# Kernel tuning notes

Measured on AMD Instinct MI355X. Metric: run time of the kernel, lower is better.

The kernel has to match this reference:

```python
import jax, jax.numpy as jnp
import numpy as np

S, B, W, H = 97, 256, 1024, 16
HD = W // H


def setup_inputs() -> dict:
    key = jax.random.key(0)
    ks = jax.random.split(key, 16)
    def p(k, shape):
        return jax.random.normal(k, shape, jnp.float32) * 0.02
    return {
        "tensor": jax.random.normal(ks[0], (S, B, W), jnp.float32),
        "mask": jnp.zeros((S, S), jnp.float32),
        "q_w": p(ks[1], (W, W)), "q_b": p(ks[2], (W,)),
        "k_w": p(ks[3], (W, W)), "k_b": p(ks[4], (W,)),
        "v_w": p(ks[5], (W, W)), "v_b": p(ks[6], (W,)),
        "in_proj_w": p(ks[7], (3 * W, W)), "in_proj_b": p(ks[8], (3 * W,)),
        "mha_out_w": p(ks[9], (W, W)), "mha_out_b": p(ks[10], (W,)),
        "out_w": p(ks[11], (W, W)), "out_b": p(ks[12], (W,)),
    }


def _freqs_cos_sin(dim, seqlen, theta=10000.0):
    # matches precompute_freqs_cis: angle[t, j] = t / theta**(2j/dim)
    inv = 1.0 / (theta ** (jnp.arange(0, dim, 2, dtype=jnp.float32) / dim))  # (dim/2,)
    ang = jnp.arange(seqlen, dtype=jnp.float32)[:, None] * inv[None, :]      # (S, dim/2)
    return jnp.cos(ang)[:, None, :], jnp.sin(ang)[:, None, :]                # (S, 1, dim/2)


def _rotary(x, cos, sin):
    # x: (S, B, D); pairs (even, odd) along last dim form complex numbers
    s, b, d = x.shape
    xr = x.reshape(s, b, d // 2, 2)
    xe, xo = xr[..., 0], xr[..., 1]
    oe = xe * cos - xo * sin
    oo = xe * sin + xo * cos
    return jnp.stack([oe, oo], axis=-1).reshape(s, b, d)


def reference(tensor, mask, q_w, q_b, k_w, k_b, v_w, v_b,
              in_proj_w, in_proj_b, mha_out_w, mha_out_b, out_w, out_b):
    # tensor: (S, B, W) -- torch MHA default batch_first=False layout
    q = tensor @ q_w.T + q_b
    k = tensor @ k_w.T + k_b
    v = tensor @ v_w.T + v_b

    cos, sin = _freqs_cos_sin(W, S)
    q = _rotary(q, cos, sin)
    k = _rotary(k, cos, sin)

    # nn.MultiheadAttention internal in_proj (applied on top of q/k/v linears)
    Wq, Wk, Wv = in_proj_w[:W], in_proj_w[W:2 * W], in_proj_w[2 * W:]
    bq, bk, bv = in_proj_b[:W], in_proj_b[W:2 * W], in_proj_b[2 * W:]
    q = q @ Wq.T + bq
    k = k @ Wk.T + bk
    v = v @ Wv.T + bv

    def split_heads(x):  # (S,B,W) -> (B,H,S,HD)
        return x.reshape(S, B, H, HD).transpose(1, 2, 0, 3)

    qh, kh, vh = split_heads(q), split_heads(k), split_heads(v)
    scale = 1.0 / jnp.sqrt(jnp.float32(HD))
    scores = jnp.einsum('bhqd,bhkd->bhqk', qh, kh) * scale + mask  # additive float mask
    attn = jax.nn.softmax(scores, axis=-1)
    o = jnp.einsum('bhqk,bhkd->bhqd', attn, vh)      # (B,H,S,HD)
    o = o.transpose(2, 0, 1, 3).reshape(S, B, W)     # (S,B,W)
    o = o @ mha_out_w.T + mha_out_b                  # MHA out_proj
    return o @ out_w.T + out_b                       # module's final self.out
```

## Files before the change

### kernel.cpp

```cpp
#include <hip/hip_runtime.h>
#include <cstdint>
#include <cstddef>

#define S_LEN 97
#define B_DIM 256
#define W_DIM 1024
#define NH    16
#define HDIM  64
#define MROWS (S_LEN * B_DIM)

typedef unsigned short u16;
typedef __bf16 bf16x8 __attribute__((ext_vector_type(8)));
typedef float  f32x4  __attribute__((ext_vector_type(4)));

__device__ __forceinline__ u16 f2bf(float f) {
  __bf16 b = (__bf16)f;
  return __builtin_bit_cast(unsigned short, b);
}

__device__ __forceinline__ void gload16(const void* g, void* lds) {
  __builtin_amdgcn_global_load_lds(
      (const __attribute__((address_space(1))) void*)(uintptr_t)g,
      (__attribute__((address_space(3))) void*)(uint32_t)(uintptr_t)lds,
      16, 0, 0);
}

__global__ void k_misc(float* __restrict__ tab, const float* __restrict__ mask,
                       float* __restrict__ maskP, const float* __restrict__ q_b,
                       const float* __restrict__ k_b, float* __restrict__ bc1,
                       float* __restrict__ zb) {
  const int blk = blockIdx.x, t = threadIdx.x;
  if (blk < 194) {
    const int idx = blk * 256 + t;
    if (idx < S_LEN * 512) {
      const int s = idx / 512, i = idx % 512;
      const float freq = expf(-(float)i * (9.210340371976184f / 512.0f));
      float sv, cv;
      sincosf((float)s * freq, &sv, &cv);
      tab[idx * 2 + 0] = cv;
      tab[idx * 2 + 1] = sv;
    }
  } else if (blk < 258) {
    const int i = (blk - 194) * 256 + t;
    const int r = i >> 7, c = i & 127;
    float v;
    if (c >= S_LEN) v = -1e30f;
    else if (r < S_LEN) v = mask[r * S_LEN + c];
    else v = 0.f;
    maskP[i] = v;
  } else if (blk < 266) {
    const int i = (blk - 258) * 256 + t;
    bc1[i] = (i < W_DIM) ? q_b[i] : k_b[i - W_DIM];
  } else {
    const int i = (blk - 266) * 256 + t;
    zb[i] = 0.f;
  }
}

__global__ void k_wcvt(const float* __restrict__ q_w, const float* __restrict__ k_w,
                       const float* __restrict__ in_proj_w, const float* __restrict__ out_w,
                       u16* __restrict__ WC1, u16* __restrict__ W2, u16* __restrict__ WO) {
  const int i = blockIdx.x * 256 + threadIdx.x;
  const float* s; u16* d; int off;
  if (i < 262144)        { s = q_w;       d = WC1;           off = i; }
  else if (i < 524288)   { s = k_w;       d = WC1 + 1048576; off = i - 262144; }
  else if (i < 1310720)  { s = in_proj_w; d = W2;            off = i - 524288; }
  else                   { s = out_w;     d = WO;            off = i - 1310720; }
  float4 v = ((const float4*)s)[off];
  uint2 pk;
  pk.x = (uint32_t)f2bf(v.x) | ((uint32_t)f2bf(v.y) << 16);
  pk.y = (uint32_t)f2bf(v.z) | ((uint32_t)f2bf(v.w) << 16);
  ((uint2*)d)[off] = pk;
}

__global__ void k_cvt(const float* __restrict__ s, u16* __restrict__ d, int n4) {
  int i = blockIdx.x * blockDim.x + threadIdx.x;
  if (i >= n4) return;
  float4 v = ((const float4*)s)[i];
  uint2 pk;
  pk.x = (uint32_t)f2bf(v.x) | ((uint32_t)f2bf(v.y) << 16);
  pk.y = (uint32_t)f2bf(v.z) | ((uint32_t)f2bf(v.w) << 16);
  ((uint2*)d)[i] = pk;
}

__global__ void k_cvt_t2(const float* __restrict__ s0, u16* __restrict__ d0,
                         const float* __restrict__ s1, u16* __restrict__ d1) {
  __shared__ float t[32][33];
  const float* src = blockIdx.z ? s1 : s0;
  u16* dst = blockIdx.z ? d1 : d0;
  const int bx = blockIdx.x * 32, by = blockIdx.y * 32;
  const int tx = threadIdx.x, ty = threadIdx.y;
  for (int yy = ty; yy < 32; yy += 8)
    t[yy][tx] = src[(size_t)(by + yy) * 1024 + bx + tx];
  __syncthreads();
  for (int yy = ty; yy < 32; yy += 8)
    dst[(size_t)(bx + yy) * 1024 + by + tx] = f2bf(t[tx][yy]);
}

__global__ void k_biasfold2(const float* __restrict__ M0, const float* __restrict__ v0,
                            const float* __restrict__ b0, float* __restrict__ o0,
                            const float* __restrict__ M1, const float* __restrict__ v1,
                            const float* __restrict__ b1, float* __restrict__ o1) {
  const int blk = blockIdx.x;
  const int lane = threadIdx.x & 63, wave = threadIdx.x >> 6;
  const float* M; const float* v; const float* b2; float* out; int rb;
  if (blk < 256) { M = M0; v = v0; b2 = b0; out = o0; rb = blk * 4; }
  else           { M = M1; v = v1; b2 = b1; out = o1; rb = (blk - 256) * 4; }
  const int row = rb + wave;
  float s = 0.f;
  for (int k = lane; k < 1024; k += 64) s += M[(size_t)row * 1024 + k] * v[k];
#pragma unroll
  for (int d = 32; d; d >>= 1) s += __shfl_xor(s, d);
  if (lane == 0) out[row] = s + b2[row];
}

__global__ __launch_bounds__(256) void k_gemmfold(
    const u16* __restrict__ A0, const u16* __restrict__ B0, u16* __restrict__ C0,
    const u16* __restrict__ A1, const u16* __restrict__ B1, u16* __restrict__ C1,
    const float* __restrict__ zb) {
  __shared__ u16 As[128 * 64];
  __shared__ u16 Bs[128 * 64];

  const u16* A = blockIdx.z ? A1 : A0;
  const u16* Bw = blockIdx.z ? B1 : B0;
  u16* Cp = blockIdx.z ? C1 : C0;

  const int tid = threadIdx.x, lane = tid & 63, wave = tid >> 6;
  const int wm = wave >> 1, wn = wave & 1;
  const int m0 = blockIdx.y * 128;
  const int n0 = blockIdx.x * 128;

  f32x4 acc[4][4] = {};

  const int lrow = lane >> 3;
  const int lcol = (lane & 7) * 8;
  const u16* Ag = A + (size_t)(m0 + wave * 8 + lrow) * 1024 + lcol;
  const u16* Bg = Bw + (size_t)(n0 + wave * 8 + lrow) * 1024 + lcol;
  u16* Asl = As + wave * 8 * 64;
  u16* Bsl = Bs + wave * 8 * 64;

  for (int kt = 0; kt < 1024; kt += 64) {
#pragma unroll
    for (int i = 0; i < 4; ++i) {
      gload16(Ag + (size_t)(i * 32) * 1024 + kt, Asl + i * 2048);
      gload16(Bg + (size_t)(i * 32) * 1024 + kt, Bsl + i * 2048);
    }
    __syncthreads();
#pragma unroll
    for (int kk = 0; kk < 2; ++kk) {
      bf16x8 af[4], bfr[4];
#pragma unroll
      for (int m = 0; m < 4; ++m)
        af[m] = *(const bf16x8*)(As + (wm * 64 + m * 16 + (lane & 15)) * 64 + kk * 32 + (lane >> 4) * 8);
#pragma unroll
      for (int n = 0; n < 4; ++n)
        bfr[n] = *(const bf16x8*)(Bs + (wn * 64 + n * 16 + (lane & 15)) * 64 + kk * 32 + (lane >> 4) * 8);
#pragma unroll
      for (int m = 0; m < 4; ++m)
#pragma unroll
        for (int n = 0; n < 4; ++n)
          acc[m][n] = __builtin_amdgcn_mfma_f32_16x16x32_bf16(af[m], bfr[n], acc[m][n], 0, 0, 0);
    }
    __syncthreads();
  }

  const int r0 = (lane >> 4) * 4;
  const int c0 = lane & 15;
#pragma unroll
  for (int m = 0; m < 4; ++m)
#pragma unroll
    for (int n = 0; n < 4; ++n) {
      const int col = n0 + wn * 64 + n * 16 + c0;
#pragma unroll
      for (int r = 0; r < 4; ++r) {
        const int row = m0 + wm * 64 + m * 16 + r0 + r;
        Cp[(size_t)row * 1024 + col] = f2bf(acc[m][n][r] + zb[col]);
      }
    }
}

template <int MODE>
__global__ __launch_bounds__(512, 4) void k_gemm256(
    const u16* __restrict__ A, int lda,
    const u16* __restrict__ BwA, const u16* __restrict__ BwB,
    const float* __restrict__ biasA, const float* __restrict__ biasB,
    void* __restrict__ CpA, void* __restrict__ CpB, int ldc,
    size_t thirdStride, const float* __restrict__ tab, int Nt, int NtA) {
  __shared__ u16 lds[3 * 12288];

  const int tid = threadIdx.x, lane = tid & 63, wave = tid >> 6;
  const int wm = wave >> 2, wn = wave & 3;
  const int c0 = lane & 15, hi = lane >> 4;

  const int nwg = gridDim.x;
  const int qq = nwg >> 3, rr_ = nwg & 7;
  const int xcd = blockIdx.x & 7, sub = blockIdx.x >> 3;
  const int seq = (xcd < rr_ ? xcd * (qq + 1) : rr_ * (qq + 1) + (xcd - rr_) * qq) + sub;
  const int mt = seq / Nt, ntRaw = seq - mt * Nt;
  const int m0 = mt * 128;
  bool isV = false;
  int n0 = ntRaw * 256;
  const u16* Bbase;
  const float* bias;
  if (MODE == 0) {
    if (ntRaw >= NtA) {
      isV = true;
      n0 = (ntRaw - NtA) * 256;
      Bbase = BwB + (size_t)n0 * 1024;
      bias = biasB;
    } else {
      Bbase = BwA + (size_t)n0 * 1024;
      bias = biasA;
    }
  } else {
    Bbase = BwA + (size_t)n0 * 1024;
    bias = biasA;
  }
  const int aoff = (MODE == 1) ? (n0 & ~1023) : 0;

  const int Lb = tid >> 3, pc = tid & 7;
  const int lcl = pc ^ (Lb & 7);
  const int rsel = lcl >> 2;
  const int csel = (lcl & 3) * 8;
  const u16* aS = A + (size_t)(m0 + Lb + 64 * rsel) * lda + aoff + csel;
  const u16* bS0 = Bbase + (size_t)(Lb + 128 * rsel) * 1024 + csel;
  const u16* bS1 = Bbase + (size_t)(64 + Lb + 128 * rsel) * 1024 + csel;
  const uint32_t ldsW = wave * 512;

  auto stage = [&](int tt, u16* slot) {
    gload16(aS + tt * 32, slot + ldsW);
    gload16(bS0 + tt * 32, slot + 4096 + ldsW);
    gload16(bS1 + tt * 32, slot + 8192 + ldsW);
  };

  int aofr[4], bofr[4];
#pragma unroll
  for (int m = 0; m < 4; ++m)
    aofr[m] = (m * 16 + c0) * 64 + ((((wm << 2) | hi) ^ (c0 & 7)) * 8);
#pragma unroll
  for (int n = 0; n < 4; ++n)
    bofr[n] = 4096 + ((wn & 1) * 64 + n * 16 + c0) * 64 +
              (((((wn >> 1) << 2) | hi) ^ (c0 & 7)) * 8);

  u16* s0 = lds;
  u16* s1 = lds + 12288;
  u16* s2 = lds + 24576;

  stage(0, s0); stage(1, s1);
  asm volatile("s_waitcnt vmcnt(3)" ::: "memory");
  __builtin_amdgcn_s_barrier();
  __builtin_amdgcn_sched_barrier(0);

  f32x4 acc[4][4] = {};

  for (int t = 0; t < 32; ++t) {
    bf16x8 af[4], bfr[4];
#pragma unroll
    for (int n = 0; n < 4; ++n) bfr[n] = *(const bf16x8*)(s0 + bofr[n]);
#pragma unroll
    for (int m = 0; m < 4; ++m) af[m] = *(const bf16x8*)(s0 + aofr[m]);
    if (t + 2 < 32) stage(t + 2, s2);
    __builtin_amdgcn_s_setprio(1);
#pragma unroll
    for (int m = 0; m < 4; ++m)
#pragma unroll
      for (int n = 0; n < 4; ++n)
        acc[m][n] = __builtin_amdgcn_mfma_f32_16x16x32_bf16(af[m], bfr[n], acc[m][n], 0, 0, 0);
    __builtin_amdgcn_s_setprio(0);
    if (t < 31) {
      if (t < 30) asm volatile("s_waitcnt vmcnt(3)" ::: "memory");
      else        asm volatile("s_waitcnt vmcnt(0)" ::: "memory");
      __builtin_amdgcn_s_barrier();
      __builtin_amdgcn_sched_barrier(0);
      u16* tmp = s0; s0 = s1; s1 = s2; s2 = tmp;
    }
  }

  const int r0 = (lane >> 4) * 4;
#pragma unroll
  for (int m = 0; m < 4; ++m) {
#pragma unroll
    for (int n = 0; n < 4; ++n) {
      const int col = n0 + wn * 64 + n * 16 + c0;
      const float bv = bias[col];
      if (MODE == 0 && !isV) {
        const int pairI = (col & 1023) >> 1;
        const float sgn = (col & 1) ? 1.f : -1.f;
#pragma unroll
        for (int r = 0; r < 4; ++r) {
          const int row = m0 + wm * 64 + m * 16 + r0 + r;
          const float v = acc[m][n][r] + bv;
          const float p = __shfl_xor(v, 1);
          const float2 cs = ((const float2*)tab)[(row >> 8) * 512 + pairI];
          ((u16*)CpA)[(size_t)row * ldc + col] = f2bf(v * cs.x + sgn * p * cs.y);
        }
      } else if (MODE == 0 && isV) {
        const int h = (col >> 6) & 15, d = col & 63;
#pragma unroll
        for (int r = 0; r < 4; ++r) {
          const int row = m0 + wm * 64 + m * 16 + r0 + r;
          const int s = row >> 8, b = row & 255;
          ((u16*)CpB)[(((size_t)(b * NH + h) * S_LEN + s) * HDIM + d)] =
              f2bf(acc[m][n][r] + bv);
        }
      } else if (MODE == 1) {
        const int which = col >> 10, c = col & 1023;
        const int h = c >> 6, d = c & 63;
        const float sc = (which == 0) ? 0.125f : 1.0f;
#pragma unroll
        for (int r = 0; r < 4; ++r) {
          const int row = m0 + wm * 64 + m * 16 + r0 + r;
          const int s = row >> 8, b = row & 255;
          ((u16*)CpA)[(size_t)which * thirdStride +
                      (((size_t)(b * NH + h) * S_LEN + s) * HDIM + d)] =
              f2bf((acc[m][n][r] + bv) * sc);
        }
      } else {
#pragma unroll
        for (int r = 0; r < 4; ++r) {
          const int row = m0 + wm * 64 + m * 16 + r0 + r;
          ((float*)CpA)[(size_t)row * ldc + col] = acc[m][n][r] + bv;
        }
      }
    }
  }
}

__global__ __launch_bounds__(512, 4) void k_attn(const u16* __restrict__ qkv2,
                                                 const float* __restrict__ maskP,
                                                 u16* __restrict__ O1) {
  __shared__ u16 Vt[66 * 128];
  __shared__ u16 Pb[128 * 128];
  __shared__ float redS[128];

  const size_t TS = (size_t)MROWS * W_DIM;
  const int bh = blockIdx.x, b = bh >> 4, h = bh & 15;
  const int tid = threadIdx.x, lane = tid & 63, wave = tid >> 6;
  const int wm = wave >> 2;
  const int wn = wave & 3;
  const int c0 = lane & 15, hi = lane >> 4;

  const u16* Qg = qkv2 + (size_t)bh * (S_LEN * HDIM);
  const u16* Kg = Qg + TS;
  const u16* Vg = Qg + 2 * TS;

  float mk[4][2][4];
#pragma unroll
  for (int m = 0; m < 4; ++m)
#pragma unroll
    for (int n = 0; n < 2; ++n)
#pragma unroll
      for (int r = 0; r < 4; ++r)
        mk[m][n][r] = maskP[(wm * 64 + m * 16 + hi * 4 + r) * 128 + wn * 32 + n * 16 + c0];

  for (int idx = tid; idx < 1024; idx += 512) {
    const int s = idx >> 3, c = (idx & 7) * 8;
    uint4 vv = make_uint4(0, 0, 0, 0);
    if (s < S_LEN) vv = *(const uint4*)(Vg + (size_t)s * HDIM + c);
    u16 tmp[8];
    *(uint4*)tmp = vv;
#pragma unroll
    for (int j = 0; j < 8; ++j)
      Vt[(c + j) * 128 + (s ^ (j << 3))] = tmp[j];
  }
  if (tid < 128) Vt[64 * 128 + tid] = 0x3F80;

  f32x4 acc[4][2] = {};
#pragma unroll
  for (int kk = 0; kk < 2; ++kk) {
    bf16x8 af[4], bfr[2];
#pragma unroll
    for (int m = 0; m < 4; ++m)
      af[m] = *(const bf16x8*)(Qg + (size_t)(wm * 64 + m * 16 + c0) * HDIM + kk * 32 + hi * 8);
#pragma unroll
    for (int n = 0; n < 2; ++n)
      bfr[n] = *(const bf16x8*)(Kg + (size_t)(wn * 32 + n * 16 + c0) * HDIM + kk * 32 + hi * 8);
#pragma unroll
    for (int m = 0; m < 4; ++m)
#pragma unroll
      for (int n = 0; n < 2; ++n)
        acc[m][n] = __builtin_amdgcn_mfma_f32_16x16x32_bf16(af[m], bfr[n], acc[m][n], 0, 0, 0);
  }

#pragma unroll
  for (int m = 0; m < 4; ++m) {
#pragma unroll
    for (int r = 0; r < 4; ++r) {
      const int row = wm * 64 + m * 16 + hi * 4 + r;
#pragma unroll
      for (int n = 0; n < 2; ++n) {
        const int col = wn * 32 + n * 16 + c0;
        const float e = __expf(acc[m][n][r] + mk[m][n][r]);
        Pb[row * 128 + (col ^ ((row & 7) << 3))] = f2bf(e);
      }
    }
  }
  __syncthreads();

  f32x4 o[4] = {};
  f32x4 osum[4] = {};
#pragma unroll
  for (int kk = 0; kk < 4; ++kk) {
    bf16x8 pa[4], vb, vbs;
#pragma unroll
    for (int m = 0; m < 4; ++m) {
      const int row = wm * 64 + m * 16 + c0;
      pa[m] = *(const bf16x8*)(Pb + row * 128 + ((kk * 32 + hi * 8) ^ ((row & 7) << 3)));
    }
    {
      const int d = wn * 16 + c0;
      vb = *(const bf16x8*)(Vt + d * 128 + ((kk * 32 + hi * 8) ^ ((d & 7) << 3)));
    }
    if (wn == 0)
      vbs = *(const bf16x8*)(Vt + 64 * 128 + (kk * 32 + hi * 8));
#pragma unroll
    for (int m = 0; m < 4; ++m)
      o[m] = __builtin_amdgcn_mfma_f32_16x16x32_bf16(pa[m], vb, o[m], 0, 0, 0);
    if (wn == 0) {
#pragma unroll
      for (int m = 0; m < 4; ++m)
        osum[m] = __builtin_amdgcn_mfma_f32_16x16x32_bf16(pa[m], vbs, osum[m], 0, 0, 0);
    }
  }

  if (wn == 0 && c0 == 0) {
#pragma unroll
    for (int m = 0; m < 4; ++m)
#pragma unroll
      for (int r = 0; r < 4; ++r)
        redS[wm * 64 + m * 16 + hi * 4 + r] = osum[m][r];
  }
  __syncthreads();

  u16* Ob = Pb;
#pragma unroll
  for (int m = 0; m < 4; ++m)
#pragma unroll
    for (int r = 0; r < 4; ++r) {
      const int row = wm * 64 + m * 16 + hi * 4 + r;
      const float iv = 1.0f / redS[row];
      Ob[row * 80 + wn * 16 + c0] = f2bf(o[m][r] * iv);
    }
  __syncthreads();

  if (tid < 4 * S_LEN) {
    const int row = tid >> 2, q = tid & 3;
    const u16* src = Ob + row * 80 + q * 16;
    uint4 a0 = *(const uint4*)(src);
    uint4 a1 = *(const uint4*)(src + 8);
    u16* dst = O1 + ((size_t)row * B_DIM + b) * W_DIM + h * HDIM + q * 16;
    *(uint4*)dst = a0;
    *(uint4*)(dst + 8) = a1;
  }
}

extern "C" void kernel_launch(void* const* d_in, const int* in_sizes, int n_in,
                              void* d_out, int out_size, void* d_ws, size_t ws_size,
                              hipStream_t stream) {
  (void)in_sizes; (void)n_in; (void)out_size; (void)ws_size;
  const float* tensor    = (const float*)d_in[0];
  const float* mask      = (const float*)d_in[1];
  const float* q_w       = (const float*)d_in[2];
  const float* q_b       = (const float*)d_in[3];
  const float* k_w       = (const float*)d_in[4];
  const float* k_b       = (const float*)d_in[5];
  const float* v_w       = (const float*)d_in[6];
  const float* v_b       = (const float*)d_in[7];
  const float* in_proj_w = (const float*)d_in[8];
  const float* in_proj_b = (const float*)d_in[9];
  const float* mha_w     = (const float*)d_in[10];
  const float* mha_b     = (const float*)d_in[11];
  const float* out_w     = (const float*)d_in[12];
  const float* out_b     = (const float*)d_in[13];

  char* ws = (char*)d_ws;
  size_t off = 0;
  auto alloc = [&](size_t bytes) {
    char* p = ws + off;
    off += (bytes + 255) & ~(size_t)255;
    return p;
  };

  const size_t TS = (size_t)MROWS * W_DIM;

  float* tab = (float*)alloc((size_t)S_LEN * 512 * 2 * sizeof(float));
  float* maskP = (float*)alloc((size_t)128 * 128 * sizeof(float));
  u16* Xbf   = (u16*)alloc(TS * 2);
  u16* qkv1  = (u16*)alloc((size_t)MROWS * 2048 * 2);
  u16* qkv2  = (u16*)alloc(TS * 3 * 2);
  u16* WC1   = (u16*)alloc((size_t)2048 * 1024 * 2);
  u16* W2    = (u16*)alloc((size_t)3072 * 1024 * 2);
  u16* WvT   = (u16*)alloc((size_t)1024 * 1024 * 2);
  u16* WmT   = (u16*)alloc((size_t)1024 * 1024 * 2);
  u16* WO    = (u16*)alloc((size_t)1024 * 1024 * 2);
  u16* WVf   = (u16*)alloc((size_t)1024 * 1024 * 2);
  u16* WFf   = (u16*)alloc((size_t)1024 * 1024 * 2);
  float* bc1 = (float*)alloc(2048 * sizeof(float));
  float* bvf = (float*)alloc(1024 * sizeof(float));
  float* bff = (float*)alloc(1024 * sizeof(float));
  float* zb  = (float*)alloc(1024 * sizeof(float));
  u16* O1 = Xbf;

  k_misc<<<dim3(270), 256, 0, stream>>>(tab, mask, maskP, q_b, k_b, bc1, zb);
  k_wcvt<<<dim3(6144), 256, 0, stream>>>(q_w, k_w, in_proj_w, out_w, WC1, W2, WO);
  k_cvt_t2<<<dim3(32, 32, 2), dim3(32, 8), 0, stream>>>(v_w, WvT, mha_w, WmT);
  k_biasfold2<<<dim3(512), 256, 0, stream>>>(
      in_proj_w + (size_t)2048 * 1024, v_b, in_proj_b + 2048, bvf,
      out_w, mha_b, out_b, bff);
  k_cvt<<<dim3(MROWS * W_DIM / 4 / 256), 256, 0, stream>>>(tensor, Xbf, MROWS * W_DIM / 4);

  k_gemmfold<<<dim3(8, 8, 2), 256, 0, stream>>>(
      W2 + (size_t)2048 * 1024, WvT, WVf, WO, WmT, WFf, zb);

  k_gemm256<0><<<dim3(194 * 12), 512, 0, stream>>>(
      Xbf, W_DIM, WC1, WVf, bc1, bvf, qkv1, qkv2 + 2 * TS, 2048, TS, tab, 12, 8);

  k_gemm256<1><<<dim3(194 * 8), 512, 0, stream>>>(
      qkv1, 2048, W2, nullptr, in_proj_b, nullptr, qkv2, nullptr, 0, TS, nullptr, 8, 0);

  k_attn<<<dim3(B_DIM * NH), 512, 0, stream>>>(qkv2, maskP, O1);

  k_gemm256<2><<<dim3(194 * 4), 512, 0, stream>>>(
      O1, W_DIM, WFf, nullptr, bff, nullptr, d_out, nullptr, W_DIM, 0, nullptr, 4, 0);
}
```

Measured before the change: 520.6 us.

## Merge prep kernels into one launch and compute softmax sums via shuffles

Five preprocessing kernels (input cast, weight casts, transposed weight casts, bias folding, rotary table/mask setup) are merged into a single launch with a block-index dispatch, cutting launch overhead and gaps between kernels. In attention, the row sums for softmax normalisation are now computed from the fp32 exponentials with lane shuffles and a small per-wave LDS array, instead of an extra MFMA against a column of ones. The mask is read from global memory inside the exp loop rather than preloaded into registers, and the launch bound is raised to 6 waves per SIMD to lift occupancy, which risks register spills.

Result: no change. 523.4 us (+0.5%).

```diff
diff --git a/kernel.cpp b/kernel.cpp
--- a/kernel.cpp
+++ b/kernel.cpp
@@ -25,93 +25,94 @@
       16, 0, 0);
 }
 
-__global__ void k_misc(float* __restrict__ tab, const float* __restrict__ mask,
+__global__ void k_prep(const float* __restrict__ tensor, u16* __restrict__ Xbf,
+                       const float* __restrict__ q_w, const float* __restrict__ k_w,
+                       const float* __restrict__ in_proj_w, const float* __restrict__ out_w,
+                       u16* __restrict__ WC1, u16* __restrict__ W2, u16* __restrict__ WO,
+                       const float* __restrict__ v_w, u16* __restrict__ WvT,
+                       const float* __restrict__ mha_w, u16* __restrict__ WmT,
+                       const float* __restrict__ v_b, const float* __restrict__ in_proj_b,
+                       float* __restrict__ bvf,
+                       const float* __restrict__ mha_b, const float* __restrict__ out_b,
+                       float* __restrict__ bff,
+                       float* __restrict__ tab, const float* __restrict__ mask,
                        float* __restrict__ maskP, const float* __restrict__ q_b,
                        const float* __restrict__ k_b, float* __restrict__ bc1,
                        float* __restrict__ zb) {
+  __shared__ float tlds[32][33];
   const int blk = blockIdx.x, t = threadIdx.x;
-  if (blk < 194) {
-    const int idx = blk * 256 + t;
-    if (idx < S_LEN * 512) {
-      const int s = idx / 512, i = idx % 512;
-      const float freq = expf(-(float)i * (9.210340371976184f / 512.0f));
-      float sv, cv;
-      sincosf((float)s * freq, &sv, &cv);
-      tab[idx * 2 + 0] = cv;
-      tab[idx * 2 + 1] = sv;
-    }
-  } else if (blk < 258) {
-    const int i = (blk - 194) * 256 + t;
-    const int r = i >> 7, c = i & 127;
-    float v;
-    if (c >= S_LEN) v = -1e30f;
-    else if (r < S_LEN) v = mask[r * S_LEN + c];
-    else v = 0.f;
-    maskP[i] = v;
-  } else if (blk < 266) {
-    const int i = (blk - 258) * 256 + t;
-    bc1[i] = (i < W_DIM) ? q_b[i] : k_b[i - W_DIM];
+
+  if (blk < 24832) {
+    const int i = blk * 256 + t;
+    float4 v = ((const float4*)tensor)[i];
+    uint2 pk;
+    pk.x = (uint32_t)f2bf(v.x) | ((uint32_t)f2bf(v.y) << 16);
+    pk.y = (uint32_t)f2bf(v.z) | ((uint32_t)f2bf(v.w) << 16);
+    ((uint2*)Xbf)[i] = pk;
+  } else if (blk < 30976) {
+    const int i = (blk - 24832) * 256 + t;
+    const float* s; u16* d; int off;
+    if (i < 262144)        { s = q_w;       d = WC1;           off = i; }
+    else if (i < 524288)   { s = k_w;       d = WC1 + 1048576; off = i - 262144; }
+    else if (i < 1310720)  { s = in_proj_w; d = W2;            off = i - 524288; }
+    else                   { s = out_w;     d = WO;            off = i - 1310720; }
+    float4 v = ((const float4*)s)[off];
+    uint2 pk;
+    pk.x = (uint32_t)f2bf(v.x) | ((uint32_t)f2bf(v.y) << 16);
+    pk.y = (uint32_t)f2bf(v.z) | ((uint32_t)f2bf(v.w) << 16);
+    ((uint2*)d)[off] = pk;
+  } else if (blk < 33024) {
+    const int idx = blk - 30976;
+    const int z = idx >> 10, rem = idx & 1023;
+    const float* src = z ? mha_w : v_w;
+    u16* dst = z ? WmT : WvT;
+    const int bx = (rem & 31) * 32, by = (rem >> 5) * 32;
+    const int tx = t & 31, ty = t >> 5;
+    for (int yy = ty; yy < 32; yy += 8)
+      tlds[yy][tx] = src[(size_t)(by + yy) * 1024 + bx + tx];
+    __syncthreads();
+    for (int yy = ty; yy < 32; yy += 8)
+      dst[(size_t)(bx + yy) * 1024 + by + tx] = f2bf(tlds[tx][yy]);
+  } else if (blk < 33536) {
+    const int bb = blk - 33024;
+    const int lane = t & 63, wave = t >> 6;
+    const float* M; const float* v; const float* b2; float* out; int rb;
+    if (bb < 256) { M = in_proj_w + (size_t)2048 * 1024; v = v_b; b2 = in_proj_b + 2048; out = bvf; rb = bb * 4; }
+    else          { M = out_w; v = mha_b; b2 = out_b; out = bff; rb = (bb - 256) * 4; }
+    const int row = rb + wave;
+    float s = 0.f;
+    for (int k = lane; k < 1024; k += 64) s += M[(size_t)row * 1024 + k] * v[k];
+#pragma unroll
+    for (int d = 32; d; d >>= 1) s += __shfl_xor(s, d);
+    if (lane == 0) out[row] = s + b2[row];
   } else {
-    const int i = (blk - 266) * 256 + t;
-    zb[i] = 0.f;
-  }
-}
-
-__global__ void k_wcvt(const float* __restrict__ q_w, const float* __restrict__ k_w,
-                       const float* __restrict__ in_proj_w, const float* __restrict__ out_w,
-                       u16* __restrict__ WC1, u16* __restrict__ W2, u16* __restrict__ WO) {
-  const int i = blockIdx.x * 256 + threadIdx.x;
-  const float* s; u16* d; int off;
-  if (i < 262144)        { s = q_w;       d = WC1;           off = i; }
-  else if (i < 524288)   { s = k_w;       d = WC1 + 1048576; off = i - 262144; }
-  else if (i < 1310720)  { s = in_proj_w; d = W2;            off = i - 524288; }
-  else                   { s = out_w;     d = WO;            off = i - 1310720; }
-  float4 v = ((const float4*)s)[off];
-  uint2 pk;
-  pk.x = (uint32_t)f2bf(v.x) | ((uint32_t)f2bf(v.y) << 16);
-  pk.y = (uint32_t)f2bf(v.z) | ((uint32_t)f2bf(v.w) << 16);
-  ((uint2*)d)[off] = pk;
-}
-
-__global__ void k_cvt(const float* __restrict__ s, u16* __restrict__ d, int n4) {
-  int i = blockIdx.x * blockDim.x + threadIdx.x;
-  if (i >= n4) return;
-  float4 v = ((const float4*)s)[i];
-  uint2 pk;
-  pk.x = (uint32_t)f2bf(v.x) | ((uint32_t)f2bf(v.y) << 16);
-  pk.y = (uint32_t)f2bf(v.z) | ((uint32_t)f2bf(v.w) << 16);
-  ((uint2*)d)[i] = pk;
-}
-
-__global__ void k_cvt_t2(const float* __restrict__ s0, u16* __restrict__ d0,
-                         const float* __restrict__ s1, u16* __restrict__ d1) {
-  __shared__ float t[32][33];
-  const float* src = blockIdx.z ? s1 : s0;
-  u16* dst = blockIdx.z ? d1 : d0;
-  const int bx = blockIdx.x * 32, by = blockIdx.y * 32;
-  const int tx = threadIdx.x, ty = threadIdx.y;
-  for (int yy = ty; yy < 32; yy += 8)
-    t[yy][tx] = src[(size_t)(by + yy) * 1024 + bx + tx];
-  __syncthreads();
-  for (int yy = ty; yy < 32; yy += 8)
-    dst[(size_t)(bx + yy) * 1024 + by + tx] = f2bf(t[tx][yy]);
-}
-
-__global__ void k_biasfold2(const float* __restrict__ M0, const float* __restrict__ v0,
-                            const float* __restrict__ b0, float* __restrict__ o0,
-                            const float* __restrict__ M1, const float* __restrict__ v1,
-                            const float* __restrict__ b1, float* __restrict__ o1) {
-  const int blk = blockIdx.x;
-  const int lane = threadIdx.x & 63, wave = threadIdx.x >> 6;
-  const float* M; const float* v; const float* b2; float* out; int rb;
-  if (blk < 256) { M = M0; v = v0; b2 = b0; out = o0; rb = blk * 4; }
-  else           { M = M1; v = v1; b2 = b1; out = o1; rb = (blk - 256) * 4; }
-  const int row = rb + wave;
-  float s = 0.f;
-  for (int k = lane; k < 1024; k += 64) s += M[(size_t)row * 1024 + k] * v[k];
-#pragma unroll
-  for (int d = 32; d; d >>= 1) s += __shfl_xor(s, d);
-  if (lane == 0) out[row] = s + b2[row];
+    const int bb = blk - 33536;
+    if (bb < 194) {
+      const int idx = bb * 256 + t;
+      if (idx < S_LEN * 512) {
+        const int s = idx / 512, i = idx % 512;
+        const float freq = expf(-(float)i * (9.210340371976184f / 512.0f));
+        float sv, cv;
+        sincosf((float)s * freq, &sv, &cv);
+        tab[idx * 2 + 0] = cv;
+        tab[idx * 2 + 1] = sv;
+      }
+    } else if (bb < 258) {
+      const int i = (bb - 194) * 256 + t;
+      const int r = i >> 7, c = i & 127;
+      float v;
+      if (c >= S_LEN) v = -1e30f;
+      else if (r < S_LEN) v = mask[r * S_LEN + c];
+      else v = 0.f;
+      maskP[i] = v;
+    } else if (bb < 266) {
+      const int i = (bb - 258) * 256 + t;
+      bc1[i] = (i < W_DIM) ? q_b[i] : k_b[i - W_DIM];
+    } else {
+      const int i = (bb - 266) * 256 + t;
+      zb[i] = 0.f;
+    }
+  }
 }
 
 __global__ __launch_bounds__(256) void k_gemmfold(
@@ -326,12 +327,12 @@
   }
 }
 
-__global__ __launch_bounds__(512, 4) void k_attn(const u16* __restrict__ qkv2,
+__global__ __launch_bounds__(512, 6) void k_attn(const u16* __restrict__ qkv2,
                                                  const float* __restrict__ maskP,
                                                  u16* __restrict__ O1) {
-  __shared__ u16 Vt[66 * 128];
+  __shared__ u16 Vt[64 * 128];
   __shared__ u16 Pb[128 * 128];
-  __shared__ float redS[128];
+  __shared__ float redS[4][128];
 
   const size_t TS = (size_t)MROWS * W_DIM;
   const int bh = blockIdx.x, b = bh >> 4, h = bh & 15;
@@ -344,15 +345,6 @@
   const u16* Kg = Qg + TS;
   const u16* Vg = Qg + 2 * TS;
 
-  float mk[4][2][4];
-#pragma unroll
-  for (int m = 0; m < 4; ++m)
-#pragma unroll
-    for (int n = 0; n < 2; ++n)
-#pragma unroll
-      for (int r = 0; r < 4; ++r)
-        mk[m][n][r] = maskP[(wm * 64 + m * 16 + hi * 4 + r) * 128 + wn * 32 + n * 16 + c0];
-
   for (int idx = tid; idx < 1024; idx += 512) {
     const int s = idx >> 3, c = (idx & 7) * 8;
     uint4 vv = make_uint4(0, 0, 0, 0);
@@ -363,7 +355,6 @@
     for (int j = 0; j < 8; ++j)
       Vt[(c + j) * 128 + (s ^ (j << 3))] = tmp[j];
   }
-  if (tid < 128) Vt[64 * 128 + tid] = 0x3F80;
 
   f32x4 acc[4][2] = {};
 #pragma unroll
@@ -384,24 +375,37 @@
 
 #pragma unroll
   for (int m = 0; m < 4; ++m) {
+    float psm[4];
 #pragma unroll
     for (int r = 0; r < 4; ++r) {
       const int row = wm * 64 + m * 16 + hi * 4 + r;
+      float p = 0.f;
 #pragma unroll
       for (int n = 0; n < 2; ++n) {
         const int col = wn * 32 + n * 16 + c0;
-        const float e = __expf(acc[m][n][r] + mk[m][n][r]);
+        const float e = __expf(acc[m][n][r] + maskP[row * 128 + col]);
+        p += e;
         Pb[row * 128 + (col ^ ((row & 7) << 3))] = f2bf(e);
       }
+      psm[r] = p;
+    }
+#pragma unroll
+    for (int d = 1; d < 16; d <<= 1)
+#pragma unroll
+      for (int r = 0; r < 4; ++r)
+        psm[r] += __shfl_xor(psm[r], d);
+    if (c0 == 0) {
+#pragma unroll
+      for (int r = 0; r < 4; ++r)
+        redS[wn][wm * 64 + m * 16 + hi * 4 + r] = psm[r];
     }
   }
   __syncthreads();
 
   f32x4 o[4] = {};
-  f32x4 osum[4] = {};
 #pragma unroll
   for (int kk = 0; kk < 4; ++kk) {
-    bf16x8 pa[4], vb, vbs;
+    bf16x8 pa[4], vb;
 #pragma unroll
     for (int m = 0; m < 4; ++m) {
       const int row = wm * 64 + m * 16 + c0;
@@ -411,24 +415,9 @@
       const int d = wn * 16 + c0;
       vb = *(const bf16x8*)(Vt + d * 128 + ((kk * 32 + hi * 8) ^ ((d & 7) << 3)));
     }
-    if (wn == 0)
-      vbs = *(const bf16x8*)(Vt + 64 * 128 + (kk * 32 + hi * 8));
 #pragma unroll
     for (int m = 0; m < 4; ++m)
       o[m] = __builtin_amdgcn_mfma_f32_16x16x32_bf16(pa[m], vb, o[m], 0, 0, 0);
-    if (wn == 0) {
-#pragma unroll
-      for (int m = 0; m < 4; ++m)
-        osum[m] = __builtin_amdgcn_mfma_f32_16x16x32_bf16(pa[m], vbs, osum[m], 0, 0, 0);
-    }
-  }
-
-  if (wn == 0 && c0 == 0) {
-#pragma unroll
-    for (int m = 0; m < 4; ++m)
-#pragma unroll
-      for (int r = 0; r < 4; ++r)
-        redS[wm * 64 + m * 16 + hi * 4 + r] = osum[m][r];
   }
   __syncthreads();
 
@@ -438,7 +427,7 @@
 #pragma unroll
     for (int r = 0; r < 4; ++r) {
       const int row = wm * 64 + m * 16 + hi * 4 + r;
-      const float iv = 1.0f / redS[row];
+      const float iv = 1.0f / (redS[0][row] + redS[1][row] + redS[2][row] + redS[3][row]);
       Ob[row * 80 + wn * 16 + c0] = f2bf(o[m][r] * iv);
     }
   __syncthreads();
@@ -501,13 +490,10 @@
   float* zb  = (float*)alloc(1024 * sizeof(float));
   u16* O1 = Xbf;
 
-  k_misc<<<dim3(270), 256, 0, stream>>>(tab, mask, maskP, q_b, k_b, bc1, zb);
-  k_wcvt<<<dim3(6144), 256, 0, stream>>>(q_w, k_w, in_proj_w, out_w, WC1, W2, WO);
-  k_cvt_t2<<<dim3(32, 32, 2), dim3(32, 8), 0, stream>>>(v_w, WvT, mha_w, WmT);
-  k_biasfold2<<<dim3(512), 256, 0, stream>>>(
-      in_proj_w + (size_t)2048 * 1024, v_b, in_proj_b + 2048, bvf,
-      out_w, mha_b, out_b, bff);
-  k_cvt<<<dim3(MROWS * W_DIM / 4 / 256), 256, 0, stream>>>(tensor, Xbf, MROWS * W_DIM / 4);
+  k_prep<<<dim3(33806), 256, 0, stream>>>(
+      tensor, Xbf, q_w, k_w, in_proj_w, out_w, WC1, W2, WO,
+      v_w, WvT, mha_w, WmT, v_b, in_proj_b, bvf, mha_b, out_b, bff,
+      tab, mask, maskP, q_b, k_b, bc1, zb);
 
   k_gemmfold<<<dim3(8, 8, 2), 256, 0, stream>>>(
       W2 + (size_t)2048 * 1024, WvT, WVf, WO, WmT, WFf, zb);
```
